# Kernel optimization log

Measured on AMD Instinct MI355X. Metric: run time of the kernel, lower is better.

## Reference

```python
import jax, jax.numpy as jnp
import numpy as np

N_EMBED = 1024
N_HEADS = 16
HEAD_DIM = N_EMBED // N_HEADS


def setup_inputs() -> dict:
    key = jax.random.key(0)
    ks = jax.random.split(key, 5)
    x = jax.random.normal(ks[0], (4, 2048, N_EMBED), dtype=jnp.float32)
    # Linear params (torch nn.Linear: y = x @ W.T + b); store W as [in, out]
    s = 1.0 / np.sqrt(N_EMBED)
    W_attn = jax.random.uniform(ks[1], (N_EMBED, 3 * N_EMBED), minval=-s, maxval=s, dtype=jnp.float32)
    b_attn = jax.random.uniform(ks[2], (3 * N_EMBED,), minval=-s, maxval=s, dtype=jnp.float32)
    W_proj = jax.random.uniform(ks[3], (N_EMBED, N_EMBED), minval=-s, maxval=s, dtype=jnp.float32)
    b_proj = jax.random.uniform(ks[4], (N_EMBED,), minval=-s, maxval=s, dtype=jnp.float32)
    return {"x": x, "W_attn": W_attn, "b_attn": b_attn, "W_proj": W_proj, "b_proj": b_proj}


def reference(x, W_attn, b_attn, W_proj, b_proj):
    B, L, D = x.shape
    H, Hd = N_HEADS, HEAD_DIM
    qkv = x @ W_attn + b_attn  # [B, L, 3D]
    q, k, v = jnp.split(qkv, 3, axis=-1)
    q = q.reshape(B, L, H, Hd).transpose(0, 2, 1, 3)  # [B, H, L, Hd]
    k = k.reshape(B, L, H, Hd).transpose(0, 2, 1, 3)
    v = v.reshape(B, L, H, Hd).transpose(0, 2, 1, 3)
    scores = jnp.einsum('bhqd,bhkd->bhqk', q, k) / jnp.sqrt(jnp.float32(Hd))
    causal = jnp.tril(jnp.ones((L, L), dtype=bool))
    scores = jnp.where(causal[None, None], scores, -jnp.inf)
    probs = jax.nn.softmax(scores.astype(jnp.float32), axis=-1).astype(x.dtype)
    o = jnp.einsum('bhqk,bhkd->bhqd', probs, v)  # [B, H, L, Hd]
    o = o.transpose(0, 2, 1, 3).reshape(B, L, D)
    return o @ W_proj + b_proj
```

## Files before the change

kernel.cpp:

```cpp
#include <hip/hip_runtime.h>


typedef __attribute__((ext_vector_type(8))) short short8;
typedef __attribute__((ext_vector_type(4))) float f32x4;

#define DEVI __device__ __forceinline__

constexpr int NE = 1024, NH = 16, NB = 4, L = 2048;
constexpr int M = NB * L;
constexpr int KD = 1024;

DEVI unsigned short f2bf(float f) {
    union { float f; unsigned u; } v; v.f = f;
    unsigned u = v.u;
    u += 0x7fffu + ((u >> 16) & 1u);
    return (unsigned short)(u >> 16);
}

typedef const __attribute__((address_space(1))) void* gas_t;
typedef __attribute__((address_space(3))) void* las_t;
DEVI void gl_lds16(const void* g, void* l) {
    __builtin_amdgcn_global_load_lds((gas_t)g, (las_t)l, 16, 0, 0);
}

__global__ void k_f32_to_bf16(const float* __restrict__ in,
                              unsigned short* __restrict__ out, int n8) {
    int i = blockIdx.x * blockDim.x + threadIdx.x;
    if (i >= n8) return;
    const float4* p = (const float4*)in + (size_t)i * 2;
    float4 a = p[0], b = p[1];
    short8 r;
    r[0] = f2bf(a.x); r[1] = f2bf(a.y); r[2] = f2bf(a.z); r[3] = f2bf(a.w);
    r[4] = f2bf(b.x); r[5] = f2bf(b.y); r[6] = f2bf(b.z); r[7] = f2bf(b.w);
    ((short8*)out)[i] = r;
}

__global__ void k_transpose_bf16(const float* __restrict__ in,
                                 unsigned short* __restrict__ out, int R, int C) {
    __shared__ float t[32][33];
    int x = blockIdx.x * 32 + threadIdx.x;
    int y0 = blockIdx.y * 32;
#pragma unroll
    for (int i = 0; i < 4; i++)
        t[threadIdx.y + 8 * i][threadIdx.x] = in[(size_t)(y0 + threadIdx.y + 8 * i) * C + x];
    __syncthreads();
    int xo = y0 + threadIdx.x;
    int yo = blockIdx.x * 32 + threadIdx.y;
#pragma unroll
    for (int i = 0; i < 4; i++)
        out[(size_t)(yo + 8 * i) * R + xo] = f2bf(t[threadIdx.x][threadIdx.y + 8 * i]);
}

template <int MODE>
__global__ __launch_bounds__(256, 2)
void k_gemm(const unsigned short* __restrict__ A,
            const unsigned short* __restrict__ Bt,
            const float* __restrict__ bias,
            unsigned short* __restrict__ Qb,
            unsigned short* __restrict__ Kb,
            unsigned short* __restrict__ Vt,
            float* __restrict__ out) {
    __shared__ alignas(16) short As[128 * 32];
    __shared__ alignas(16) short Bs[128 * 32];
    const int tid = threadIdx.x;
    const int lane = tid & 63, wid = tid >> 6;
    const int quad = lane >> 4, l16 = lane & 15;
    const int wm = (wid >> 1) * 64, wn = (wid & 1) * 64;
    const int m0 = blockIdx.y * 128;
    const int n0 = blockIdx.x * 128;

    const int srow = lane >> 2, sseg = lane & 3;

    f32x4 acc[4][4] = {};

    for (int kk = 0; kk < KD; kk += 32) {
        __syncthreads();
#pragma unroll
        for (int c = 0; c < 2; c++) {
            const int rbase = c * 64 + wid * 16;
            gl_lds16(&A[(size_t)(m0 + rbase + srow) * KD + kk + sseg * 8], &As[rbase * 32]);
            gl_lds16(&Bt[(size_t)(n0 + rbase + srow) * KD + kk + sseg * 8], &Bs[rbase * 32]);
        }
        __syncthreads();
        short8 af[4], bf[4];
#pragma unroll
        for (int t = 0; t < 4; t++) {
            af[t] = *(const short8*)&As[(wm + t * 16 + l16) * 32 + quad * 8];
            bf[t] = *(const short8*)&Bs[(wn + t * 16 + l16) * 32 + quad * 8];
        }
#pragma unroll
        for (int mt = 0; mt < 4; mt++)
#pragma unroll
            for (int nt = 0; nt < 4; nt++)
                acc[mt][nt] = __builtin_amdgcn_mfma_f32_16x16x32_bf16(
                    af[mt], bf[nt], acc[mt][nt], 0, 0, 0);
    }

#pragma unroll
    for (int nt = 0; nt < 4; nt++) {
        const int n = n0 + wn + nt * 16 + l16;
        const float bv = bias[n];
        if (MODE == 0) {
            const int sel = n >> 10;
            const int h = (n & 1023) >> 6;
            const int d = n & 63;
#pragma unroll
            for (int mt = 0; mt < 4; mt++)
#pragma unroll
                for (int r = 0; r < 4; r++) {
                    const int m = m0 + wm + mt * 16 + quad * 4 + r;
                    const int b = m >> 11, l = m & 2047;
                    const int bh = b * NH + h;
                    const float v = acc[mt][nt][r] + bv;
                    if (sel == 0)      Qb[(size_t)(bh * L + l) * 64 + d] = f2bf(v * 0.125f);
                    else if (sel == 1) Kb[(size_t)(bh * L + l) * 64 + d] = f2bf(v);
                    else               Vt[(size_t)(bh * 64 + d) * L + l] = f2bf(v);
                }
        } else {
#pragma unroll
            for (int mt = 0; mt < 4; mt++)
#pragma unroll
                for (int r = 0; r < 4; r++) {
                    const int m = m0 + wm + mt * 16 + quad * 4 + r;
                    out[(size_t)m * NE + n] = acc[mt][nt][r] + bv;
                }
        }
    }
}

__global__ __launch_bounds__(256, 2)
void k_attn(const unsigned short* __restrict__ Q,
            const unsigned short* __restrict__ Kb,
            const unsigned short* __restrict__ Vt,
            unsigned short* __restrict__ O) {
    __shared__ alignas(16) short Ks[128 * 64];
    __shared__ alignas(16) short Vs[64 * 128];
    __shared__ alignas(16) short Ps[4][32][36];

    const int tid = threadIdx.x;
    const int lane = tid & 63, wid = tid >> 6;
    const int quad = lane >> 4, l16 = lane & 15;
    const int bh = blockIdx.x;
    const int qb = (int)(gridDim.y - 1) - (int)blockIdx.y;
    const int q0 = qb * 128 + wid * 32;
    const size_t base = (size_t)bh * L * 64;

    short8 qf[2][2];
#pragma unroll
    for (int mt = 0; mt < 2; mt++)
#pragma unroll
        for (int dc = 0; dc < 2; dc++)
            qf[mt][dc] = *(const short8*)&Q[base + (size_t)(q0 + mt * 16 + l16) * 64 + dc * 32 + quad * 8];

    f32x4 o[2][4] = {};
    float lrow[2][4] = {};

    const int nlim_diag = wid * 2 + 2;

    for (int kt = 0; kt <= qb; kt++) {
        __syncthreads();
#pragma unroll
        for (int c = 0; c < 4; c++) {
            const int row = c * 32 + wid * 8 + (lane >> 3);
            const int gseg = (lane & 7) ^ (row & 7);
            gl_lds16(&Kb[base + (size_t)(kt * 128 + row) * 64 + gseg * 8],
                     &Ks[(c * 32 + wid * 8) * 64]);
        }
#pragma unroll
        for (int c = 0; c < 4; c++) {
            const int row = c * 16 + wid * 4 + (lane >> 4);
            const int gseg = (lane & 15) ^ (row & 15);
            gl_lds16(&Vt[base + (size_t)row * L + kt * 128 + gseg * 8],
                     &Vs[(c * 16 + wid * 4) * 128]);
        }
        __syncthreads();

        const bool diag = (kt == qb);
        const int chunks = diag ? (nlim_diag >> 1) : 4;

        for (int kc = 0; kc < chunks; kc++) {
            f32x4 sA[2][2];
#pragma unroll
            for (int j = 0; j < 2; j++) {
                const int R = (kc * 2 + j) * 16 + l16;
                short8 kf0 = *(const short8*)&Ks[R * 64 + ((quad ^ (R & 7)) * 8)];
                short8 kf1 = *(const short8*)&Ks[R * 64 + (((4 + quad) ^ (R & 7)) * 8)];
#pragma unroll
                for (int mt = 0; mt < 2; mt++) {
                    f32x4 z = {};
                    z = __builtin_amdgcn_mfma_f32_16x16x32_bf16(qf[mt][0], kf0, z, 0, 0, 0);
                    z = __builtin_amdgcn_mfma_f32_16x16x32_bf16(qf[mt][1], kf1, z, 0, 0, 0);
                    sA[mt][j] = z;
                }
            }
#pragma unroll
            for (int mt = 0; mt < 2; mt++)
#pragma unroll
                for (int r = 0; r < 4; r++) {
                    const int q = q0 + mt * 16 + quad * 4 + r;
                    float p0 = __expf(sA[mt][0][r]);
                    float p1 = __expf(sA[mt][1][r]);
                    if (diag) {
                        const int col = kt * 128 + kc * 32 + l16;
                        if (col > q) p0 = 0.f;
                        if (col + 16 > q) p1 = 0.f;
                    }
                    lrow[mt][r] += p0 + p1;
                    const int prow = mt * 16 + quad * 4 + r;
                    Ps[wid][prow][l16] = (short)f2bf(p0);
                    Ps[wid][prow][16 + l16] = (short)f2bf(p1);
                }
#pragma unroll
            for (int mt = 0; mt < 2; mt++) {
                short8 pf = *(const short8*)&Ps[wid][mt * 16 + l16][quad * 8];
#pragma unroll
                for (int dt = 0; dt < 4; dt++) {
                    const int R2 = dt * 16 + l16;
                    short8 vf = *(const short8*)&Vs[R2 * 128 + (((kc * 4 + quad) ^ (R2 & 15)) * 8)];
                    o[mt][dt] = __builtin_amdgcn_mfma_f32_16x16x32_bf16(pf, vf, o[mt][dt], 0, 0, 0);
                }
            }
        }
    }

    const int b = bh >> 4, h = bh & 15;
#pragma unroll
    for (int mt = 0; mt < 2; mt++)
#pragma unroll
        for (int r = 0; r < 4; r++) {
            float rs = lrow[mt][r];
            rs += __shfl_xor(rs, 1);
            rs += __shfl_xor(rs, 2);
            rs += __shfl_xor(rs, 4);
            rs += __shfl_xor(rs, 8);
            const float inv = 1.0f / rs;
            const int q = q0 + mt * 16 + quad * 4 + r;
#pragma unroll
            for (int dt = 0; dt < 4; dt++)
                O[(size_t)(b * L + q) * NE + h * 64 + dt * 16 + l16] = f2bf(o[mt][dt][r] * inv);
        }
}

extern "C" void kernel_launch(void* const* d_in, const int* in_sizes, int n_in,
                              void* d_out, int out_size, void* d_ws, size_t ws_size,
                              hipStream_t stream) {
    const float* x  = (const float*)d_in[0];
    const float* Wa = (const float*)d_in[1];
    const float* ba = (const float*)d_in[2];
    const float* Wp = (const float*)d_in[3];
    const float* bp = (const float*)d_in[4];
    float* out = (float*)d_out;

    char* ws = (char*)d_ws;
    unsigned short* xb  = (unsigned short*)(ws);
    unsigned short* WaT = (unsigned short*)(ws + (16u << 20));
    unsigned short* WpT = (unsigned short*)(ws + (22u << 20));
    unsigned short* Qb  = (unsigned short*)(ws + (24u << 20));
    unsigned short* Kb  = (unsigned short*)(ws + (40u << 20));
    unsigned short* Vt  = (unsigned short*)(ws + (56u << 20));

    k_f32_to_bf16<<<(M * NE / 8 + 255) / 256, 256, 0, stream>>>(x, xb, M * NE / 8);
    k_transpose_bf16<<<dim3(3 * NE / 32, NE / 32), dim3(32, 8), 0, stream>>>(Wa, WaT, NE, 3 * NE);
    k_transpose_bf16<<<dim3(NE / 32, NE / 32), dim3(32, 8), 0, stream>>>(Wp, WpT, NE, NE);

    k_gemm<0><<<dim3(3 * NE / 128, M / 128), 256, 0, stream>>>(xb, WaT, ba, Qb, Kb, Vt, nullptr);

    unsigned short* Ob = xb;
    k_attn<<<dim3(NB * NH, L / 128), 256, 0, stream>>>(Qb, Kb, Vt, Ob);

    k_gemm<1><<<dim3(NE / 128, M / 128), 256, 0, stream>>>(Ob, WpT, bp, nullptr, nullptr, nullptr, out);
}
```

Baseline: 275.4 us.

## Deepen GEMM K-tile with swizzled LDS and restructure attention with transposed MFMA

The GEMM now stages 64-wide K tiles with an XOR swizzle, which halves the barrier count per output tile. The attention kernel pairs causal query blocks (qb and 15-qb) inside one workgroup to balance the triangular workload, and halves the grid. It computes S^T so probabilities stay in registers as MFMA operands, which removes the P round trip through LDS, and it loads V through registers into padded LDS. The output is staged through LDS so stores to global memory are coalesced. The risks are lower parallelism from the smaller grid and extra register pressure.

```diff
diff --git a/kernel.cpp b/kernel.cpp
--- a/kernel.cpp
+++ b/kernel.cpp
@@ -2,6 +2,7 @@
 
 
 typedef __attribute__((ext_vector_type(8))) short short8;
+typedef __attribute__((ext_vector_type(4))) short s16x4;
 typedef __attribute__((ext_vector_type(4))) float f32x4;
 
 #define DEVI __device__ __forceinline__
@@ -10,11 +11,11 @@
 constexpr int M = NB * L;
 constexpr int KD = 1024;
 
-DEVI unsigned short f2bf(float f) {
+DEVI unsigned f2bf(float f) {
     union { float f; unsigned u; } v; v.f = f;
     unsigned u = v.u;
     u += 0x7fffu + ((u >> 16) & 1u);
-    return (unsigned short)(u >> 16);
+    return u >> 16;
 }
 
 typedef const __attribute__((address_space(1))) void* gas_t;
@@ -60,8 +61,8 @@
             unsigned short* __restrict__ Kb,
             unsigned short* __restrict__ Vt,
             float* __restrict__ out) {
-    __shared__ alignas(16) short As[128 * 32];
-    __shared__ alignas(16) short Bs[128 * 32];
+    __shared__ alignas(16) short As[128 * 64];
+    __shared__ alignas(16) short Bs[128 * 64];
     const int tid = threadIdx.x;
     const int lane = tid & 63, wid = tid >> 6;
     const int quad = lane >> 4, l16 = lane & 15;
@@ -69,31 +70,37 @@
     const int m0 = blockIdx.y * 128;
     const int n0 = blockIdx.x * 128;
 
-    const int srow = lane >> 2, sseg = lane & 3;
+    const int srow = lane >> 3;
+    const int gseg = (lane & 7) ^ srow;
 
     f32x4 acc[4][4] = {};
 
-    for (int kk = 0; kk < KD; kk += 32) {
+    for (int kk = 0; kk < KD; kk += 64) {
         __syncthreads();
 #pragma unroll
-        for (int c = 0; c < 2; c++) {
-            const int rbase = c * 64 + wid * 16;
-            gl_lds16(&A[(size_t)(m0 + rbase + srow) * KD + kk + sseg * 8], &As[rbase * 32]);
-            gl_lds16(&Bt[(size_t)(n0 + rbase + srow) * KD + kk + sseg * 8], &Bs[rbase * 32]);
+        for (int c = 0; c < 4; c++) {
+            const int rbase = c * 32 + wid * 8;
+            gl_lds16(&A[(size_t)(m0 + rbase + srow) * KD + kk + gseg * 8], &As[rbase * 64]);
+            gl_lds16(&Bt[(size_t)(n0 + rbase + srow) * KD + kk + gseg * 8], &Bs[rbase * 64]);
         }
         __syncthreads();
-        short8 af[4], bf[4];
-#pragma unroll
-        for (int t = 0; t < 4; t++) {
-            af[t] = *(const short8*)&As[(wm + t * 16 + l16) * 32 + quad * 8];
-            bf[t] = *(const short8*)&Bs[(wn + t * 16 + l16) * 32 + quad * 8];
-        }
-#pragma unroll
-        for (int mt = 0; mt < 4; mt++)
-#pragma unroll
-            for (int nt = 0; nt < 4; nt++)
-                acc[mt][nt] = __builtin_amdgcn_mfma_f32_16x16x32_bf16(
-                    af[mt], bf[nt], acc[mt][nt], 0, 0, 0);
+#pragma unroll
+        for (int kc = 0; kc < 2; kc++) {
+            short8 af[4], bf[4];
+#pragma unroll
+            for (int t = 0; t < 4; t++) {
+                const int Ra = wm + t * 16 + l16;
+                af[t] = *(const short8*)&As[Ra * 64 + (((kc * 4 + quad) ^ (Ra & 7)) * 8)];
+                const int Rb = wn + t * 16 + l16;
+                bf[t] = *(const short8*)&Bs[Rb * 64 + (((kc * 4 + quad) ^ (Rb & 7)) * 8)];
+            }
+#pragma unroll
+            for (int mt = 0; mt < 4; mt++)
+#pragma unroll
+                for (int nt = 0; nt < 4; nt++)
+                    acc[mt][nt] = __builtin_amdgcn_mfma_f32_16x16x32_bf16(
+                        af[mt], bf[nt], acc[mt][nt], 0, 0, 0);
+        }
     }
 
 #pragma unroll
@@ -133,112 +140,140 @@
             const unsigned short* __restrict__ Kb,
             const unsigned short* __restrict__ Vt,
             unsigned short* __restrict__ O) {
-    __shared__ alignas(16) short Ks[128 * 64];
-    __shared__ alignas(16) short Vs[64 * 128];
-    __shared__ alignas(16) short Ps[4][32][36];
+    __shared__ alignas(16) short smem[16896];
+    short* Ks = smem;
+    short* Vs = smem + 8192;
+    short* Os = smem;
 
     const int tid = threadIdx.x;
     const int lane = tid & 63, wid = tid >> 6;
     const int quad = lane >> 4, l16 = lane & 15;
     const int bh = blockIdx.x;
-    const int qb = (int)(gridDim.y - 1) - (int)blockIdx.y;
-    const int q0 = qb * 128 + wid * 32;
+    const int pr = blockIdx.y;
     const size_t base = (size_t)bh * L * 64;
-
-    short8 qf[2][2];
-#pragma unroll
-    for (int mt = 0; mt < 2; mt++)
-#pragma unroll
-        for (int dc = 0; dc < 2; dc++)
-            qf[mt][dc] = *(const short8*)&Q[base + (size_t)(q0 + mt * 16 + l16) * 64 + dc * 32 + quad * 8];
-
-    f32x4 o[2][4] = {};
-    float lrow[2][4] = {};
-
-    const int nlim_diag = wid * 2 + 2;
-
-    for (int kt = 0; kt <= qb; kt++) {
-        __syncthreads();
-#pragma unroll
-        for (int c = 0; c < 4; c++) {
-            const int row = c * 32 + wid * 8 + (lane >> 3);
-            const int gseg = (lane & 7) ^ (row & 7);
-            gl_lds16(&Kb[base + (size_t)(kt * 128 + row) * 64 + gseg * 8],
-                     &Ks[(c * 32 + wid * 8) * 64]);
-        }
-#pragma unroll
-        for (int c = 0; c < 4; c++) {
-            const int row = c * 16 + wid * 4 + (lane >> 4);
-            const int gseg = (lane & 15) ^ (row & 15);
-            gl_lds16(&Vt[base + (size_t)row * L + kt * 128 + gseg * 8],
-                     &Vs[(c * 16 + wid * 4) * 128]);
-        }
-        __syncthreads();
-
-        const bool diag = (kt == qb);
-        const int chunks = diag ? (nlim_diag >> 1) : 4;
-
-        for (int kc = 0; kc < chunks; kc++) {
-            f32x4 sA[2][2];
-#pragma unroll
-            for (int j = 0; j < 2; j++) {
-                const int R = (kc * 2 + j) * 16 + l16;
-                short8 kf0 = *(const short8*)&Ks[R * 64 + ((quad ^ (R & 7)) * 8)];
-                short8 kf1 = *(const short8*)&Ks[R * 64 + (((4 + quad) ^ (R & 7)) * 8)];
+    const int b = bh >> 4, h = bh & 15;
+
+    const int srow = lane >> 3;
+    const int gsegK = (lane & 7) ^ srow;
+
+    for (int phase = 0; phase < 2; phase++) {
+        const int qb = phase ? pr : 15 - pr;
+        const int q0 = qb * 128 + wid * 32;
+
+        short8 qf[2][2];
+#pragma unroll
+        for (int mt = 0; mt < 2; mt++)
+#pragma unroll
+            for (int dc = 0; dc < 2; dc++)
+                qf[mt][dc] = *(const short8*)&Q[base + (size_t)(q0 + mt * 16 + l16) * 64 + dc * 32 + quad * 8];
+
+        f32x4 o[2][4] = {};
+        float lrow[2] = {0.f, 0.f};
+
+        for (int kt = 0; kt <= qb; kt++) {
+            __syncthreads();
+#pragma unroll
+            for (int c = 0; c < 4; c++) {
+                const int rbase = c * 32 + wid * 8;
+                gl_lds16(&Kb[base + (size_t)(kt * 128 + rbase + srow) * 64 + gsegK * 8],
+                         &Ks[rbase * 64]);
+            }
+            short8 vtmp[4];
+            const int vd = lane >> 4, vseg = lane & 15;
+#pragma unroll
+            for (int c = 0; c < 4; c++)
+                vtmp[c] = *(const short8*)&Vt[base + (size_t)(c * 16 + wid * 4 + vd) * L + kt * 128 + vseg * 8];
+#pragma unroll
+            for (int c = 0; c < 4; c++)
+                *(short8*)&Vs[(c * 16 + wid * 4 + vd) * 136 + vseg * 8] = vtmp[c];
+            __syncthreads();
+
+            const bool diag = (kt == qb);
+            const int chunks = diag ? (wid + 1) : 4;
+
+            for (int kc = 0; kc < chunks; kc++) {
+                short8 kf[2][2];
+#pragma unroll
+                for (int j0 = 0; j0 < 2; j0++)
+#pragma unroll
+                    for (int dc = 0; dc < 2; dc++) {
+                        const int R = kc * 32 + j0 * 16 + l16;
+                        kf[j0][dc] = *(const short8*)&Ks[R * 64 + (((dc * 4 + quad) ^ (R & 7)) * 8)];
+                    }
+                f32x4 st[2][2];
+#pragma unroll
+                for (int mt = 0; mt < 2; mt++)
+#pragma unroll
+                    for (int j0 = 0; j0 < 2; j0++) {
+                        f32x4 z = {};
+                        z = __builtin_amdgcn_mfma_f32_16x16x32_bf16(kf[j0][0], qf[mt][0], z, 0, 0, 0);
+                        z = __builtin_amdgcn_mfma_f32_16x16x32_bf16(kf[j0][1], qf[mt][1], z, 0, 0, 0);
+                        st[mt][j0] = z;
+                    }
+                const bool dm = diag && (kc == wid);
+                short8 pb[2];
 #pragma unroll
                 for (int mt = 0; mt < 2; mt++) {
-                    f32x4 z = {};
-                    z = __builtin_amdgcn_mfma_f32_16x16x32_bf16(qf[mt][0], kf0, z, 0, 0, 0);
-                    z = __builtin_amdgcn_mfma_f32_16x16x32_bf16(qf[mt][1], kf1, z, 0, 0, 0);
-                    sA[mt][j] = z;
+                    float sum = 0.f;
+#pragma unroll
+                    for (int j0 = 0; j0 < 2; j0++)
+#pragma unroll
+                        for (int r = 0; r < 4; r++) {
+                            float pe = __expf(st[mt][j0][r]);
+                            if (dm) {
+                                const int krel = j0 * 16 + quad * 4 + r;
+                                const int qrel = mt * 16 + l16;
+                                if (krel > qrel) pe = 0.f;
+                            }
+                            sum += pe;
+                            pb[mt][j0 * 4 + r] = (short)f2bf(pe);
+                        }
+                    lrow[mt] += sum;
+                }
+#pragma unroll
+                for (int dt = 0; dt < 4; dt++) {
+                    const int va = (dt * 16 + l16) * 136 + kc * 32 + quad * 4;
+                    s16x4 lo = *(const s16x4*)&Vs[va];
+                    s16x4 hi = *(const s16x4*)&Vs[va + 16];
+                    short8 vf = __builtin_shufflevector(lo, hi, 0, 1, 2, 3, 4, 5, 6, 7);
+#pragma unroll
+                    for (int mt = 0; mt < 2; mt++)
+                        o[mt][dt] = __builtin_amdgcn_mfma_f32_16x16x32_bf16(
+                            vf, pb[mt], o[mt][dt], 0, 0, 0);
                 }
             }
-#pragma unroll
-            for (int mt = 0; mt < 2; mt++)
-#pragma unroll
-                for (int r = 0; r < 4; r++) {
-                    const int q = q0 + mt * 16 + quad * 4 + r;
-                    float p0 = __expf(sA[mt][0][r]);
-                    float p1 = __expf(sA[mt][1][r]);
-                    if (diag) {
-                        const int col = kt * 128 + kc * 32 + l16;
-                        if (col > q) p0 = 0.f;
-                        if (col + 16 > q) p1 = 0.f;
-                    }
-                    lrow[mt][r] += p0 + p1;
-                    const int prow = mt * 16 + quad * 4 + r;
-                    Ps[wid][prow][l16] = (short)f2bf(p0);
-                    Ps[wid][prow][16 + l16] = (short)f2bf(p1);
-                }
-#pragma unroll
-            for (int mt = 0; mt < 2; mt++) {
-                short8 pf = *(const short8*)&Ps[wid][mt * 16 + l16][quad * 8];
-#pragma unroll
-                for (int dt = 0; dt < 4; dt++) {
-                    const int R2 = dt * 16 + l16;
-                    short8 vf = *(const short8*)&Vs[R2 * 128 + (((kc * 4 + quad) ^ (R2 & 15)) * 8)];
-                    o[mt][dt] = __builtin_amdgcn_mfma_f32_16x16x32_bf16(pf, vf, o[mt][dt], 0, 0, 0);
-                }
+        }
+
+        float inv[2];
+#pragma unroll
+        for (int mt = 0; mt < 2; mt++) {
+            float rs = lrow[mt];
+            rs += __shfl_xor(rs, 16);
+            rs += __shfl_xor(rs, 32);
+            inv[mt] = 1.0f / rs;
+        }
+
+        __syncthreads();
+#pragma unroll
+        for (int mt = 0; mt < 2; mt++) {
+            const int ql = wid * 32 + mt * 16 + l16;
+#pragma unroll
+            for (int dt = 0; dt < 4; dt++) {
+                unsigned w0 = f2bf(o[mt][dt][0] * inv[mt]) | (f2bf(o[mt][dt][1] * inv[mt]) << 16);
+                unsigned w1 = f2bf(o[mt][dt][2] * inv[mt]) | (f2bf(o[mt][dt][3] * inv[mt]) << 16);
+                *(uint2*)&Os[ql * 72 + dt * 16 + quad * 4] = make_uint2(w0, w1);
             }
         }
+        __syncthreads();
+#pragma unroll
+        for (int i = 0; i < 4; i++) {
+            const int id = i * 256 + tid;
+            const int row = id >> 3, seg = id & 7;
+            short8 v = *(const short8*)&Os[row * 72 + seg * 8];
+            const int q = qb * 128 + row;
+            *(short8*)&O[(size_t)(b * L + q) * NE + h * 64 + seg * 8] = v;
+        }
     }
-
-    const int b = bh >> 4, h = bh & 15;
-#pragma unroll
-    for (int mt = 0; mt < 2; mt++)
-#pragma unroll
-        for (int r = 0; r < 4; r++) {
-            float rs = lrow[mt][r];
-            rs += __shfl_xor(rs, 1);
-            rs += __shfl_xor(rs, 2);
-            rs += __shfl_xor(rs, 4);
-            rs += __shfl_xor(rs, 8);
-            const float inv = 1.0f / rs;
-            const int q = q0 + mt * 16 + quad * 4 + r;
-#pragma unroll
-            for (int dt = 0; dt < 4; dt++)
-                O[(size_t)(b * L + q) * NE + h * 64 + dt * 16 + l16] = f2bf(o[mt][dt][r] * inv);
-        }
 }
 
 extern "C" void kernel_launch(void* const* d_in, const int* in_sizes, int n_in,
@@ -266,7 +301,7 @@
     k_gemm<0><<<dim3(3 * NE / 128, M / 128), 256, 0, stream>>>(xb, WaT, ba, Qb, Kb, Vt, nullptr);
 
     unsigned short* Ob = xb;
-    k_attn<<<dim3(NB * NH, L / 128), 256, 0, stream>>>(Qb, Kb, Vt, Ob);
+    k_attn<<<dim3(NB * NH, 8), 256, 0, stream>>>(Qb, Kb, Vt, Ob);
 
     k_gemm<1><<<dim3(NE / 128, M / 128), 256, 0, stream>>>(Ob, WpT, bp, nullptr, nullptr, nullptr, out);
 }
```

Measured after the change: 267.7 us. 1.03x faster.
